# Optimization experiments

Measured on AMD Instinct MI355X. Metric: run time of the kernel, lower is better.

The kernel has to match this reference:

```python
import jax, jax.numpy as jnp
import numpy as np

B, S, DIM, H, DH, DEPTH, NCLS = 4, 2048, 128, 8, 128, 2, 10
M = 128          # number of FAVOR+ random features
CHUNK = 128      # chunk size for causal linear attention
INNER = H * DH   # performer-pytorch: dim_head=dim -> inner_dim = heads*dim
FF = 4 * DIM


def layernorm(x, g, b, eps=1e-5):
    mu = jnp.mean(x, axis=-1, keepdims=True)
    var = jnp.mean((x - mu) ** 2, axis=-1, keepdims=True)
    return (x - mu) * jax.lax.rsqrt(var + eps) * g + b


def softmax_kernel(data, proj, is_query, eps=1e-4):
    # FAVOR+ positive softmax-kernel features. data: [B,H,S,DH], proj: [M,DH]
    norm = DH ** -0.25
    ratio = M ** -0.5
    d = data * norm
    dd = jnp.einsum('bhsd,md->bhsm', d, proj)
    diag = 0.5 * jnp.sum(d * d, axis=-1, keepdims=True)
    if is_query:
        stab = jnp.max(dd, axis=-1, keepdims=True)
    else:
        stab = jnp.max(dd, axis=(-2, -1), keepdims=True)
    stab = jax.lax.stop_gradient(stab)
    return ratio * (jnp.exp(dd - diag - stab) + eps)


def causal_linear_attention(qp, kp, v):
    # qp,kp: [B,H,S,M], v: [B,H,S,DH]; chunked prefix-sum causal linear attention
    b, h, s, m = qp.shape
    d = v.shape[-1]
    nc = s // CHUNK
    def to_chunks(t):
        return t.reshape(b, h, nc, CHUNK, -1).transpose(2, 0, 1, 3, 4)
    qc, kc, vc = to_chunks(qp), to_chunks(kp), to_chunks(v)
    tri = jnp.tril(jnp.ones((CHUNK, CHUNK), qp.dtype))
    def step(carry, inp):
        kv_sum, k_sum = carry           # [b,h,m,d], [b,h,m]
        qi, ki, vi = inp                # [b,h,CHUNK,*]
        attn = jnp.einsum('bhim,bhjm->bhij', qi, ki) * tri
        num = jnp.einsum('bhij,bhjd->bhid', attn, vi) \
            + jnp.einsum('bhim,bhmd->bhid', qi, kv_sum)
        den = jnp.sum(attn, axis=-1) + jnp.einsum('bhim,bhm->bhi', qi, k_sum)
        out = num / (den[..., None] + 1e-6)
        kv_sum = kv_sum + jnp.einsum('bhjm,bhjd->bhmd', ki, vi)
        k_sum = k_sum + jnp.sum(ki, axis=2)
        return (kv_sum, k_sum), out
    init = (jnp.zeros((b, h, m, d), qp.dtype), jnp.zeros((b, h, m), qp.dtype))
    _, out = jax.lax.scan(step, init, (qc, kc, vc))
    return out.transpose(1, 2, 0, 3, 4).reshape(b, h, s, d)


def setup_inputs():
    key = jax.random.key(0)
    ks = jax.random.split(key, 12)
    rng = np.random.default_rng(0)
    # sinusoidal positional encoding [S, DIM]
    pe = np.zeros((S, DIM), np.float32)
    pos = np.arange(S)[:, None].astype(np.float32)
    div = np.exp(np.arange(0, DIM, 2).astype(np.float32) * (-np.log(10000.0) / DIM))
    pe[:, 0::2] = np.sin(pos * div)
    pe[:, 1::2] = np.cos(pos * div)
    # orthogonal random feature projections per layer [DEPTH, M, DH]
    proj = np.stack([
        (np.linalg.qr(rng.standard_normal((DH, DH)))[0][:M] * np.sqrt(DH))
        for _ in range(DEPTH)
    ]).astype(np.float32)
    def gn(k, shape, scale):
        return jax.random.normal(k, shape, jnp.float32) * scale
    return {
        'x': gn(ks[0], (B, S, 1), 1.0),
        'lin_w': gn(ks[1], (1, DIM), 1.0),
        'lin_b': jnp.zeros((DIM,), jnp.float32),
        'pe': jnp.asarray(pe),
        'proj': jnp.asarray(proj),
        'ln1_g': jnp.ones((DEPTH, DIM), jnp.float32),
        'ln1_b': jnp.zeros((DEPTH, DIM), jnp.float32),
        'wq': gn(ks[2], (DEPTH, DIM, INNER), DIM ** -0.5),
        'wk': gn(ks[3], (DEPTH, DIM, INNER), DIM ** -0.5),
        'wv': gn(ks[4], (DEPTH, DIM, INNER), DIM ** -0.5),
        'wo': gn(ks[5], (DEPTH, INNER, DIM), INNER ** -0.5),
        'wo_b': jnp.zeros((DEPTH, DIM), jnp.float32),
        'ln2_g': jnp.ones((DEPTH, DIM), jnp.float32),
        'ln2_b': jnp.zeros((DEPTH, DIM), jnp.float32),
        'ff1_w': gn(ks[6], (DEPTH, DIM, FF), DIM ** -0.5),
        'ff1_b': jnp.zeros((DEPTH, FF), jnp.float32),
        'ff2_w': gn(ks[7], (DEPTH, FF, DIM), FF ** -0.5),
        'ff2_b': jnp.zeros((DEPTH, DIM), jnp.float32),
        'fin_w': gn(ks[8], (DIM, NCLS), DIM ** -0.5),
        'fin_b': jnp.zeros((NCLS,), jnp.float32),
    }


def reference(x, lin_w, lin_b, pe, proj, ln1_g, ln1_b, wq, wk, wv, wo, wo_b,
              ln2_g, ln2_b, ff1_w, ff1_b, ff2_w, ff2_b, fin_w, fin_b):
    h = x @ lin_w + lin_b            # [B,S,DIM]
    h = h + pe[None]
    for l in range(DEPTH):
        # --- pre-norm FAVOR+ causal self-attention ---
        y = layernorm(h, ln1_g[l], ln1_b[l])
        def split(t):  # [B,S,INNER] -> [B,H,S,DH]
            return t.reshape(B, S, H, DH).transpose(0, 2, 1, 3)
        q, k, v = split(y @ wq[l]), split(y @ wk[l]), split(y @ wv[l])
        qp = softmax_kernel(q, proj[l], True)
        kp = softmax_kernel(k, proj[l], False)
        o = causal_linear_attention(qp, kp, v)          # [B,H,S,DH]
        o = o.transpose(0, 2, 1, 3).reshape(B, S, INNER)
        h = h + (o @ wo[l] + wo_b[l])
        # --- pre-norm FFN ---
        y = layernorm(h, ln2_g[l], ln2_b[l])
        f = jax.nn.gelu(y @ ff1_w[l] + ff1_b[l]) @ ff2_w[l] + ff2_b[l]
        h = h + f
    pooled = jnp.mean(h, axis=1)     # [B,DIM]
    return pooled @ fin_w + fin_b    # [B,NCLS]
```

## Files before the change

kernel.cpp:

```cpp
#include <hip/hip_runtime.h>
#include <hip/hip_bf16.h>

#define Bb 4
#define Ss 2048
#define DIMc 128
#define Hh 8
#define DHc 128
#define Mf 128
#define CH 128
#define NCc 16
#define INNERc 1024
#define FFc 512

union F4 { float4 v; float f[4]; };
typedef unsigned short u16;

typedef __bf16 bf16x8 __attribute__((ext_vector_type(8)));
typedef float  f32x4  __attribute__((ext_vector_type(4)));

__device__ __forceinline__ unsigned fkey(float f){
  unsigned b = __float_as_uint(f);
  return (b & 0x80000000u) ? ~b : (b | 0x80000000u);
}
__device__ __forceinline__ float funkey(unsigned u){
  unsigned b = (u & 0x80000000u) ? (u & 0x7fffffffu) : ~u;
  return __uint_as_float(b);
}
__device__ __forceinline__ float gelu_f(float x){
  return 0.5f*x*(1.0f + tanhf(0.7978845608028654f*(x + 0.044715f*x*x*x)));
}
__device__ __forceinline__ u16 f2bu(float f){
  unsigned u = __float_as_uint(f);
  return (u16)((u + 0x7fffu + ((u>>16)&1u)) >> 16);
}
__device__ __forceinline__ float b2f(u16 u){
  return __uint_as_float(((unsigned)u)<<16);
}

__device__ __forceinline__ bf16x8 ldfrag(const u16* base, int row, int e){
  int byte = (row*256 + e*2) ^ ((row&7)<<4);
  return *(const bf16x8*)((const char*)base + byte);
}
__device__ __forceinline__ void stage_lin_bf(u16* dst, const u16* src, int srs, int t){
  #pragma unroll
  for(int it=0; it<8; ++it){
    int idx = t + it*256; int r = idx>>4, c8 = idx&15;
    int byte = (r*256 + c8*16) ^ ((r&7)<<4);
    *(uint4*)((char*)dst + byte) = *(const uint4*)(src + r*srs + c8*8);
  }
}
__device__ __forceinline__ void stage_lin_bf_s(u16* dst, const u16* src, int srs,
    int t, float sc, float off){
  #pragma unroll
  for(int it=0; it<8; ++it){
    int idx = t + it*256; int r = idx>>4, c8 = idx&15;
    u16 tmp[8]; *(uint4*)tmp = *(const uint4*)(src + r*srs + c8*8);
    #pragma unroll
    for(int u=0;u<8;u++) tmp[u] = f2bu(fmaf(b2f(tmp[u]), sc, off));
    int byte = (r*256 + c8*16) ^ ((r&7)<<4);
    *(uint4*)((char*)dst + byte) = *(uint4*)tmp;
  }
}
__device__ __forceinline__ void stage_lin_f32(u16* dst, const float* src, int srs, int t){
  #pragma unroll
  for(int it=0; it<8; ++it){
    int idx = t + it*256; int r = idx>>4, c8 = idx&15;
    F4 v0, v1;
    v0.v = *(const float4*)(src + r*srs + c8*8);
    v1.v = *(const float4*)(src + r*srs + c8*8 + 4);
    u16 tmp[8];
    #pragma unroll
    for(int u=0;u<4;u++){ tmp[u] = f2bu(v0.f[u]); tmp[4+u] = f2bu(v1.f[u]); }
    int byte = (r*256 + c8*16) ^ ((r&7)<<4);
    *(uint4*)((char*)dst + byte) = *(uint4*)tmp;
  }
}
__device__ __forceinline__ void stage_tr_bf(u16* dst, const u16* src, int srs, int t){
  int j0 = (t & 63)*2; int wv = t>>6;
  #pragma unroll
  for(int it=0; it<2; ++it){
    int d0 = wv*16 + it*64;
    u16 a0[16], a1[16];
    *(uint4*)&a0[0] = *(const uint4*)(src + j0*srs + d0);
    *(uint4*)&a0[8] = *(const uint4*)(src + j0*srs + d0 + 8);
    *(uint4*)&a1[0] = *(const uint4*)(src + (j0+1)*srs + d0);
    *(uint4*)&a1[8] = *(const uint4*)(src + (j0+1)*srs + d0 + 8);
    #pragma unroll
    for(int dc=0; dc<16; ++dc){
      int d = d0 + dc;
      unsigned pk = (unsigned)a0[dc] | ((unsigned)a1[dc]<<16);
      int byte = (d*256 + j0*2) ^ ((d&7)<<4);
      *(unsigned*)((char*)dst + byte) = pk;
    }
  }
}
__device__ __forceinline__ void stage_tr_bf_s(u16* dst, const u16* src, int srs,
    int t, float sc, float off){
  int j0 = (t & 63)*2; int wv = t>>6;
  #pragma unroll
  for(int it=0; it<2; ++it){
    int d0 = wv*16 + it*64;
    u16 a0[16], a1[16];
    *(uint4*)&a0[0] = *(const uint4*)(src + j0*srs + d0);
    *(uint4*)&a0[8] = *(const uint4*)(src + j0*srs + d0 + 8);
    *(uint4*)&a1[0] = *(const uint4*)(src + (j0+1)*srs + d0);
    *(uint4*)&a1[8] = *(const uint4*)(src + (j0+1)*srs + d0 + 8);
    #pragma unroll
    for(int dc=0; dc<16; ++dc){
      int d = d0 + dc;
      unsigned pk = (unsigned)f2bu(fmaf(b2f(a0[dc]), sc, off)) |
                    ((unsigned)f2bu(fmaf(b2f(a1[dc]), sc, off))<<16);
      int byte = (d*256 + j0*2) ^ ((d&7)<<4);
      *(unsigned*)((char*)dst + byte) = pk;
    }
  }
}

__device__ __forceinline__ int2 swz_tile(){
  int nx = gridDim.x;
  int nwg = gridDim.x*gridDim.y;
  int lin = blockIdx.y*nx + blockIdx.x;
  int q = nwg>>3, r = nwg&7;
  int xcd = lin&7, idx = lin>>3;
  int nl = (xcd<r) ? (xcd*(q+1)+idx) : (r*(q+1)+(xcd-r)*q+idx);
  return make_int2(nl % nx, nl / nx);
}

__global__ __launch_bounds__(64) void k_init(unsigned* kstab){
  if(threadIdx.x < 64) kstab[threadIdx.x] = 0u;
}

__global__ __launch_bounds__(256) void k_embed(const float* __restrict__ x,
    const float* __restrict__ lw, const float* __restrict__ lb,
    const float* __restrict__ pe, float* __restrict__ h){
  int idx = blockIdx.x*256 + threadIdx.x;
  int d = idx & 127; int bs = idx >> 7; int s = bs & (Ss-1);
  h[idx] = x[bs]*lw[d] + lb[d] + pe[s*DIMc + d];
}

__global__ __launch_bounds__(256) void k_ln(const float* __restrict__ in,
    const float* __restrict__ g, const float* __restrict__ bta,
    u16* __restrict__ out){
  int wave = threadIdx.x >> 6; int lane = threadIdx.x & 63;
  int row = blockIdx.x*4 + wave;
  const float* r = in + row*DIMc;
  float x1 = r[lane], x2 = r[lane+64];
  float s = x1+x2, sq = x1*x1 + x2*x2;
  #pragma unroll
  for(int m=1;m<64;m<<=1){ s += __shfl_xor(s,m,64); sq += __shfl_xor(sq,m,64); }
  float mu = s * (1.0f/128.0f);
  float var = sq*(1.0f/128.0f) - mu*mu;
  float rs = rsqrtf(var + 1e-5f);
  out[row*DIMc+lane]    = f2bu((x1-mu)*rs*g[lane]+bta[lane]);
  out[row*DIMc+lane+64] = f2bu((x2-mu)*rs*g[lane+64]+bta[lane+64]);
}

template<bool BIAS, bool GELU, bool RES, bool OBF>
__global__ __launch_bounds__(256) void k_gemm_bf(const u16* __restrict__ A,
    const float* __restrict__ Bw, const float* __restrict__ bias,
    const float* __restrict__ resid, void* __restrict__ Cp, int N, int K){
  __shared__ u16 As[64][40];
  __shared__ u16 Bs[64][40];
  int2 tt = swz_tile();
  int n0 = tt.x*64, m0 = tt.y*64;
  int t = threadIdx.x; int wid = t>>6, lane = t&63;
  int wr = wid>>1, wc = wid&1;
  int fr = lane&15, kc = lane>>4;
  f32x4 acc[2][2] = {};
  for(int k0=0; k0<K; k0+=32){
    {
      int r = t>>2, c8 = t&3;
      *(uint4*)&As[r][c8*8] = *(const uint4*)(A + (m0+r)*K + k0 + c8*8);
    }
    {
      int n = t&63, c8 = t>>6;
      u16 tmp[8];
      #pragma unroll
      for(int j=0;j<8;j++) tmp[j] = f2bu(Bw[(k0 + c8*8 + j)*N + n0 + n]);
      *(uint4*)&Bs[n][c8*8] = *(uint4*)tmp;
    }
    __syncthreads();
    bf16x8 af[2], bf[2];
    #pragma unroll
    for(int i=0;i<2;i++) af[i] = *(const bf16x8*)&As[wr*32 + i*16 + fr][kc*8];
    #pragma unroll
    for(int j=0;j<2;j++) bf[j] = *(const bf16x8*)&Bs[wc*32 + j*16 + fr][kc*8];
    #pragma unroll
    for(int i=0;i<2;i++)
      #pragma unroll
      for(int j=0;j<2;j++)
        acc[i][j] = __builtin_amdgcn_mfma_f32_16x16x32_bf16(af[i], bf[j], acc[i][j], 0, 0, 0);
    __syncthreads();
  }
  #pragma unroll
  for(int i=0;i<2;i++){
    #pragma unroll
    for(int r=0;r<4;r++){
      int row = m0 + wr*32 + i*16 + kc*4 + r;
      #pragma unroll
      for(int j=0;j<2;j++){
        int col = n0 + wc*32 + j*16 + fr;
        float val = acc[i][j][r];
        if(BIAS) val += bias[col];
        if(GELU) val = gelu_f(val);
        if(RES)  val += resid[row*N+col];
        if(OBF) ((u16*)Cp)[row*N+col] = f2bu(val);
        else    ((float*)Cp)[row*N+col] = val;
      }
    }
  }
}

template<bool ISQ>
__global__ __launch_bounds__(256) void k_featm(
    const u16* xin, u16* qout, const float* __restrict__ proj, unsigned* kstab){
  __shared__ __align__(16) u16 xs[16384];
  __shared__ __align__(16) u16 ps[16384];
  __shared__ float diag_s[128];
  __shared__ unsigned hmax[8];
  int r0 = blockIdx.x*128;
  int t = threadIdx.x; int lane = t&63, w = t>>6;
  int fr = lane&15, kc = lane>>4;
  const float norm  = 0.29730177875068026f;
  const float ratio = 0.08838834764831845f;
  if(!ISQ && t<8) hmax[t] = 0u;
  stage_lin_bf(xs, xin + (size_t)r0*128, 128, t);
  stage_lin_f32(ps, proj, 128, t);
  {
    int r = t>>1, half = t&1;
    const u16* rp = xin + (size_t)(r0+r)*128 + half*64;
    float ss = 0.f;
    #pragma unroll
    for(int u4=0; u4<8; ++u4){
      u16 tmp[8]; *(uint4*)tmp = *(const uint4*)(rp + u4*8);
      #pragma unroll
      for(int u=0;u<8;u++){ float f = b2f(tmp[u]); ss += f*f; }
    }
    ss += __shfl_xor(ss, 1, 64);
    if(half==0) diag_s[r] = 0.5f*norm*norm*ss;
  }
  __syncthreads();
  f32x4 acc[2][8] = {};
  #pragma unroll
  for(int ks=0; ks<4; ++ks){
    bf16x8 a[2];
    #pragma unroll
    for(int i=0;i<2;i++) a[i] = ldfrag(xs, w*32+i*16+fr, ks*32+kc*8);
    bf16x8 bm[8];
    #pragma unroll
    for(int cb=0;cb<8;cb++) bm[cb] = ldfrag(ps, cb*16+fr, ks*32+kc*8);
    #pragma unroll
    for(int i=0;i<2;i++)
      #pragma unroll
      for(int cb=0;cb<8;cb++)
        acc[i][cb] = __builtin_amdgcn_mfma_f32_16x16x32_bf16(a[i], bm[cb], acc[i][cb], 0,0,0);
  }
  __syncthreads();
  #pragma unroll
  for(int i=0;i<2;i++){
    #pragma unroll
    for(int r=0;r<4;r++){
      int row = w*32 + i*16 + kc*4 + r;
      float dg = diag_s[row];
      float rmax = acc[i][0][r];
      #pragma unroll
      for(int cb=1;cb<8;cb++) rmax = fmaxf(rmax, acc[i][cb][r]);
      #pragma unroll
      for(int msk=1;msk<16;msk<<=1) rmax = fmaxf(rmax, __shfl_xor(rmax, msk, 64));
      if(ISQ){
        float base = -dg - norm*rmax;
        #pragma unroll
        for(int cb=0;cb<8;cb++){
          float val = ratio*(expf(fmaf(norm, acc[i][cb][r], base)) + 1e-4f);
          int byte = (row*256 + (cb*16+fr)*2) ^ ((row&7)<<4);
          *(u16*)((char*)xs + byte) = f2bu(val);
        }
      } else {
        if(fr==0) atomicMax(&hmax[row&7], fkey(norm*rmax));
        #pragma unroll
        for(int cb=0;cb<8;cb++){
          float val = expf(fmaf(norm, acc[i][cb][r], -dg));
          int byte = (row*256 + (cb*16+fr)*2) ^ ((row&7)<<4);
          *(u16*)((char*)xs + byte) = f2bu(val);
        }
      }
    }
  }
  __syncthreads();
  #pragma unroll
  for(int it=0; it<8; ++it){
    int idx = t + it*256; int r = idx>>4, c8 = idx&15;
    int byte = (r*256 + c8*16) ^ ((r&7)<<4);
    *(uint4*)(qout + (size_t)(r0+r)*128 + c8*8) = *(uint4*)((char*)xs + byte);
  }
  if(!ISQ){
    int b = r0 >> 14;
    if(t<8) atomicMax(&kstab[b*8 + t], hmax[t]);
  }
}

__global__ __launch_bounds__(256) void k_attn1m(const u16* __restrict__ kp,
    const u16* __restrict__ v, u16* __restrict__ kvc, float* __restrict__ ksc,
    const unsigned* __restrict__ kstab){
  __shared__ __align__(16) u16 kt[16384];
  __shared__ __align__(16) u16 vt[16384];
  int bc = blockIdx.x; int c = bc&15, bh = bc>>4, b = bh>>3, hh = bh&7;
  int t = threadIdx.x; int lane = t&63, w = t>>6;
  int fr = lane&15, kc = lane>>4;
  int s0 = c*128;
  const float ratio = 0.08838834764831845f;
  float stab = funkey(kstab[bh]);
  float csc = ratio * expf(-stab);
  float reps = ratio * 1e-4f;
  const u16* kb = kp + (size_t)((b*Ss+s0)*Hh + hh)*128;
  const u16* vb = v  + (size_t)((b*Ss+s0)*Hh + hh)*128;
  stage_tr_bf_s(kt, kb, 1024, t, csc, reps);
  stage_tr_bf(vt, vb, 1024, t);
  __syncthreads();
  f32x4 acc[2][8] = {};
  f32x4 ks[2] = {};
  bf16x8 bones;
  #pragma unroll
  for(int e=0;e<8;e++) bones[e] = (fr==0) ? (__bf16)1.0f : (__bf16)0.0f;
  #pragma unroll
  for(int js=0;js<4;js++){
    bf16x8 am[2];
    #pragma unroll
    for(int i=0;i<2;i++) am[i] = ldfrag(kt, w*32+i*16+fr, js*32+kc*8);
    bf16x8 bv[8];
    #pragma unroll
    for(int cb=0;cb<8;cb++) bv[cb] = ldfrag(vt, cb*16+fr, js*32+kc*8);
    #pragma unroll
    for(int i=0;i<2;i++){
      ks[i] = __builtin_amdgcn_mfma_f32_16x16x32_bf16(am[i], bones, ks[i], 0,0,0);
      #pragma unroll
      for(int cb=0;cb<8;cb++)
        acc[i][cb] = __builtin_amdgcn_mfma_f32_16x16x32_bf16(am[i], bv[cb], acc[i][cb], 0,0,0);
    }
  }
  u16* kvb = kvc + (size_t)bc*16384;
  #pragma unroll
  for(int i=0;i<2;i++){
    #pragma unroll
    for(int r=0;r<4;r++){
      int m = w*32 + i*16 + kc*4 + r;
      #pragma unroll
      for(int cb=0;cb<8;cb++) kvb[m*128 + cb*16 + fr] = f2bu(acc[i][cb][r]);
      if(fr==0) ksc[bc*128 + m] = ks[i][r];
    }
  }
}

__global__ __launch_bounds__(256) void k_prefix(unsigned* __restrict__ kvc){
  int bh = blockIdx.x >> 5; int pos = (blockIdx.x & 31)*256 + threadIdx.x;
  int base = bh*16*8192 + pos;
  float a0 = 0.f, a1 = 0.f;
  #pragma unroll
  for(int c=0;c<16;c++){
    unsigned pk = kvc[base + c*8192];
    float x0 = b2f((u16)pk), x1 = b2f((u16)(pk>>16));
    kvc[base + c*8192] = (unsigned)f2bu(a0) | ((unsigned)f2bu(a1)<<16);
    a0 += x0; a1 += x1;
  }
}
__global__ __launch_bounds__(256) void k_prefix_ks(float* __restrict__ ksc){
  int e = blockIdx.x*256 + threadIdx.x;
  int bh = e>>7, m = e&127;
  float a = 0.f;
  #pragma unroll
  for(int c=0;c<16;c++){
    int idx = (bh*16+c)*128 + m;
    float xv = ksc[idx]; ksc[idx] = a; a += xv;
  }
}

__global__ __launch_bounds__(256) void k_attn2m(const u16* __restrict__ qp,
    const u16* __restrict__ kp, const u16* __restrict__ v,
    const u16* __restrict__ kvc, const float* __restrict__ ksc,
    u16* __restrict__ o, const unsigned* __restrict__ kstab){
  __shared__ __align__(16) u16 qs[16384];
  __shared__ __align__(16) u16 bs[16384];
  __shared__ float ksum_s[128];
  int bc = blockIdx.x; int c = bc&15, bh = bc>>4, b = bh>>3, hh = bh&7;
  int t = threadIdx.x; int lane = t&63, w = t>>6;
  int fr = lane&15, kc = lane>>4;
  int s0 = c*128;
  const float ratio = 0.08838834764831845f;
  float stab = funkey(kstab[bh]);
  float csc = ratio * expf(-stab);
  float reps = ratio * 1e-4f;
  const u16* qb = qp + (size_t)((b*Ss+s0)*Hh + hh)*128;
  const u16* kb = kp + (size_t)((b*Ss+s0)*Hh + hh)*128;
  const u16* vb = v  + (size_t)((b*Ss+s0)*Hh + hh)*128;
  const u16* kvb = kvc + (size_t)bc*16384;
  stage_lin_bf(qs, qb, 1024, t);
  stage_lin_bf_s(bs, kb, 1024, t, csc, reps);
  if(t<128) ksum_s[t] = ksc[bc*128 + t];
  __syncthreads();
  bf16x8 aq[2][4];
  #pragma unroll
  for(int i=0;i<2;i++)
    #pragma unroll
    for(int ks=0;ks<4;ks++)
      aq[i][ks] = ldfrag(qs, w*32+i*16+fr, ks*32+kc*8);
  f32x4 sacc[2][8] = {};
  #pragma unroll
  for(int ks=0;ks<4;ks++){
    bf16x8 bk[8];
    #pragma unroll
    for(int cb=0;cb<8;cb++) bk[cb] = ldfrag(bs, cb*16+fr, ks*32+kc*8);
    #pragma unroll
    for(int i=0;i<2;i++)
      #pragma unroll
      for(int cb=0;cb<8;cb++)
        sacc[i][cb] = __builtin_amdgcn_mfma_f32_16x16x32_bf16(aq[i][ks], bk[cb], sacc[i][cb], 0,0,0);
  }
  __syncthreads();
  #pragma unroll
  for(int i=0;i<2;i++){
    #pragma unroll
    for(int cb=0;cb<8;cb++){
      #pragma unroll
      for(int r=0;r<4;r++){
        int prow = w*32 + i*16 + kc*4 + r;
        int pcol = cb*16 + fr;
        float pv = (pcol > prow) ? 0.f : sacc[i][cb][r];
        int byte = (prow*256 + pcol*2) ^ ((prow&7)<<4);
        *(u16*)((char*)qs + byte) = f2bu(pv);
      }
    }
  }
  stage_tr_bf(bs, vb, 1024, t);
  __syncthreads();
  f32x4 nacc[2][8] = {};
  f32x4 dacc[2] = {};
  bf16x8 bones;
  #pragma unroll
  for(int e=0;e<8;e++) bones[e] = (fr==0) ? (__bf16)1.0f : (__bf16)0.0f;
  #pragma unroll
  for(int js=0;js<4;js++){
    bf16x8 ap[2];
    #pragma unroll
    for(int i=0;i<2;i++) ap[i] = ldfrag(qs, w*32+i*16+fr, js*32+kc*8);
    bf16x8 bv[8];
    #pragma unroll
    for(int cb=0;cb<8;cb++) bv[cb] = ldfrag(bs, cb*16+fr, js*32+kc*8);
    #pragma unroll
    for(int i=0;i<2;i++){
      dacc[i] = __builtin_amdgcn_mfma_f32_16x16x32_bf16(ap[i], bones, dacc[i], 0,0,0);
      #pragma unroll
      for(int cb=0;cb<8;cb++)
        nacc[i][cb] = __builtin_amdgcn_mfma_f32_16x16x32_bf16(ap[i], bv[cb], nacc[i][cb], 0,0,0);
    }
  }
  __syncthreads();
  stage_tr_bf(bs, kvb, 128, t);
  __syncthreads();
  #pragma unroll
  for(int ms=0;ms<4;ms++){
    bf16x8 bkv[8];
    #pragma unroll
    for(int cb=0;cb<8;cb++) bkv[cb] = ldfrag(bs, cb*16+fr, ms*32+kc*8);
    bf16x8 bks;
    #pragma unroll
    for(int e=0;e<8;e++) bks[e] = (fr==0) ? (__bf16)ksum_s[ms*32+kc*8+e] : (__bf16)0.0f;
    #pragma unroll
    for(int i=0;i<2;i++){
      dacc[i] = __builtin_amdgcn_mfma_f32_16x16x32_bf16(aq[i][ms], bks, dacc[i], 0,0,0);
      #pragma unroll
      for(int cb=0;cb<8;cb++)
        nacc[i][cb] = __builtin_amdgcn_mfma_f32_16x16x32_bf16(aq[i][ms], bkv[cb], nacc[i][cb], 0,0,0);
    }
  }
  #pragma unroll
  for(int i=0;i<2;i++){
    #pragma unroll
    for(int r=0;r<4;r++){
      float den = __shfl(dacc[i][r], lane & 48, 64);
      float inv = 1.0f/(den + 1e-6f);
      int row = w*32 + i*16 + kc*4 + r;
      u16* ob = o + (size_t)((b*Ss+s0+row)*Hh + hh)*128;
      #pragma unroll
      for(int cb=0;cb<8;cb++)
        ob[cb*16 + fr] = f2bu(nacc[i][cb][r] * inv);
    }
  }
}

__global__ __launch_bounds__(256) void k_pool(const float* __restrict__ h,
    float* __restrict__ pw){
  __shared__ float part[256];
  int blk = blockIdx.x; int b = blk>>4, c = blk&15;
  int t = threadIdx.x; int half = t>>7;
  float s = 0.f;
  int s0 = c*128 + half*64;
  for(int si=s0; si<s0+64; ++si) s += h[(b*Ss+si)*128 + (t&127)];
  part[t] = s;
  __syncthreads();
  if(t<128) pw[blk*128 + t] = part[t] + part[t+128];
}
__global__ __launch_bounds__(128) void k_cls(const float* __restrict__ pw,
    const float* __restrict__ fw, const float* __restrict__ fb,
    float* __restrict__ out){
  __shared__ float pool_s[128];
  int b = blockIdx.x; int t = threadIdx.x;
  float s = 0.f;
  for(int c=0;c<16;c++) s += pw[(b*16+c)*128 + t];
  pool_s[t] = s * (1.0f/2048.0f);
  __syncthreads();
  if(t<10){
    float a = fb[t];
    for(int d=0; d<128; ++d) a += pool_s[d]*fw[d*10+t];
    out[b*10+t] = a;
  }
}

extern "C" void kernel_launch(void* const* d_in, const int* in_sizes, int n_in,
                              void* d_out, int out_size, void* d_ws, size_t ws_size,
                              hipStream_t stream){
  (void)in_sizes; (void)n_in; (void)out_size; (void)ws_size;
  const float* x     = (const float*)d_in[0];
  const float* lin_w = (const float*)d_in[1];
  const float* lin_b = (const float*)d_in[2];
  const float* pe    = (const float*)d_in[3];
  const float* proj  = (const float*)d_in[4];
  const float* ln1_g = (const float*)d_in[5];
  const float* ln1_b = (const float*)d_in[6];
  const float* wq    = (const float*)d_in[7];
  const float* wk    = (const float*)d_in[8];
  const float* wv    = (const float*)d_in[9];
  const float* wo    = (const float*)d_in[10];
  const float* wo_b  = (const float*)d_in[11];
  const float* ln2_g = (const float*)d_in[12];
  const float* ln2_b = (const float*)d_in[13];
  const float* ff1w  = (const float*)d_in[14];
  const float* ff1b  = (const float*)d_in[15];
  const float* ff2w  = (const float*)d_in[16];
  const float* ff2b  = (const float*)d_in[17];
  const float* finw  = (const float*)d_in[18];
  const float* finb  = (const float*)d_in[19];
  float* out = (float*)d_out;

  float* ws  = (float*)d_ws;
  float* h    = ws;
  u16*  y    = (u16*)(h + 1048576);
  u16*  q    = (u16*)(h + 1048576 + 524288);
  u16*  k    = q + 8388608;
  u16*  v    = k + 8388608;
  u16*  o    = v + 8388608;
  u16*  kvc  = o + 8388608;
  float* ksc  = (float*)(kvc + 8388608);
  float* pw   = ksc + 65536;
  unsigned* kstab = (unsigned*)(pw + 8192);

  k_init<<<1,64,0,stream>>>(kstab);
  k_embed<<<4096,256,0,stream>>>(x, lin_w, lin_b, pe, h);
  for(int l=0;l<2;l++){
    const float* projl = proj + l*Mf*DHc;
    k_ln<<<2048,256,0,stream>>>(h, ln1_g + l*DIMc, ln1_b + l*DIMc, y);
    k_gemm_bf<false,false,false,true><<<dim3(16,128),256,0,stream>>>(y, wq + l*DIMc*INNERc, nullptr, nullptr, q, INNERc, DIMc);
    k_gemm_bf<false,false,false,true><<<dim3(16,128),256,0,stream>>>(y, wk + l*DIMc*INNERc, nullptr, nullptr, k, INNERc, DIMc);
    k_gemm_bf<false,false,false,true><<<dim3(16,128),256,0,stream>>>(y, wv + l*DIMc*INNERc, nullptr, nullptr, v, INNERc, DIMc);
    k_featm<true><<<512,256,0,stream>>>(q, q, projl, nullptr);
    k_featm<false><<<512,256,0,stream>>>(k, k, projl, kstab + l*32);
    k_attn1m<<<512,256,0,stream>>>(k, v, kvc, ksc, kstab + l*32);
    k_prefix<<<1024,256,0,stream>>>((unsigned*)kvc);
    k_prefix_ks<<<16,256,0,stream>>>(ksc);
    k_attn2m<<<512,256,0,stream>>>(q, k, v, kvc, ksc, o, kstab + l*32);
    k_gemm_bf<true,false,true,false><<<dim3(2,128),256,0,stream>>>(o, wo + l*INNERc*DIMc, wo_b + l*DIMc, h, h, DIMc, INNERc);
    k_ln<<<2048,256,0,stream>>>(h, ln2_g + l*DIMc, ln2_b + l*DIMc, y);
    k_gemm_bf<true,true,false,true><<<dim3(8,128),256,0,stream>>>(y, ff1w + l*DIMc*FFc, ff1b + l*FFc, nullptr, q, FFc, DIMc);
    k_gemm_bf<true,false,true,false><<<dim3(2,128),256,0,stream>>>(q, ff2w + l*FFc*DIMc, ff2b + l*DIMc, h, h, DIMc, FFc);
  }
  k_pool<<<64,256,0,stream>>>(h, pw);
  k_cls<<<4,128,0,stream>>>(pw, finw, finb, out);
}
```

Baseline: 455.9 us.

## Fuse QKV projections into one 128x128-tile GEMM and merge prefix kernels

Adds a k_gemm128 kernel with 128x128 output tiles and a full K=128 slab staged once in LDS. It computes Q, K and V in a single launch by selecting the weight and output per column tile, and it also replaces the FF1 GEMM (with bias and GELU). The two prefix-sum kernels are merged into one launch, cutting launch count and improving A-tile reuse. The costs are larger shared memory per block (64KB), which may lower occupancy, and strided fp32 weight loads converted to bf16 inside the kernel.

```diff
diff --git a/kernel.cpp b/kernel.cpp
--- a/kernel.cpp
+++ b/kernel.cpp
@@ -153,6 +153,70 @@
   float rs = rsqrtf(var + 1e-5f);
   out[row*DIMc+lane]    = f2bu((x1-mu)*rs*g[lane]+bta[lane]);
   out[row*DIMc+lane+64] = f2bu((x2-mu)*rs*g[lane+64]+bta[lane+64]);
+}
+
+template<bool QKV3, bool BIAS, bool GELU>
+__global__ __launch_bounds__(256) void k_gemm128(const u16* __restrict__ A,
+    const float* __restrict__ B0, const float* __restrict__ B1,
+    const float* __restrict__ B2, const float* __restrict__ bias,
+    u16* __restrict__ C0, u16* __restrict__ C1, u16* __restrict__ C2,
+    int N){
+  __shared__ __align__(16) u16 As[16384];
+  __shared__ __align__(16) u16 Bs[16384];
+  int2 tt = swz_tile();
+  int tn = tt.x, m0 = tt.y*128;
+  const float* Bw; u16* C; int n0;
+  if(QKV3){
+    int tpw = N>>7;
+    int widx = tn / tpw; n0 = (tn % tpw)*128;
+    Bw = (widx==0) ? B0 : ((widx==1) ? B1 : B2);
+    C  = (widx==0) ? C0 : ((widx==1) ? C1 : C2);
+  } else { Bw = B0; C = C0; n0 = tn*128; }
+  int t = threadIdx.x; int lane = t&63, w = t>>6;
+  int fr = lane&15, kc = lane>>4;
+  stage_lin_bf(As, A + (size_t)m0*128, 128, t);
+  {
+    #pragma unroll
+    for(int it=0; it<8; ++it){
+      int idx = t + it*256; int n = idx&127, c8 = idx>>7;
+      u16 tmp[8];
+      #pragma unroll
+      for(int j=0;j<8;j++) tmp[j] = f2bu(Bw[(c8*8+j)*N + n0 + n]);
+      int byte = (n*256 + c8*16) ^ ((n&7)<<4);
+      *(uint4*)((char*)Bs + byte) = *(uint4*)tmp;
+    }
+  }
+  __syncthreads();
+  f32x4 acc[2][8] = {};
+  #pragma unroll
+  for(int ks=0; ks<4; ++ks){
+    bf16x8 a[2];
+    #pragma unroll
+    for(int i=0;i<2;i++) a[i] = ldfrag(As, w*32+i*16+fr, ks*32+kc*8);
+    bf16x8 bm[8];
+    #pragma unroll
+    for(int cb=0;cb<8;cb++) bm[cb] = ldfrag(Bs, cb*16+fr, ks*32+kc*8);
+    #pragma unroll
+    for(int i=0;i<2;i++)
+      #pragma unroll
+      for(int cb=0;cb<8;cb++)
+        acc[i][cb] = __builtin_amdgcn_mfma_f32_16x16x32_bf16(a[i], bm[cb], acc[i][cb], 0,0,0);
+  }
+  #pragma unroll
+  for(int i=0;i<2;i++){
+    #pragma unroll
+    for(int r=0;r<4;r++){
+      int row = m0 + w*32 + i*16 + kc*4 + r;
+      #pragma unroll
+      for(int cb=0;cb<8;cb++){
+        int col = n0 + cb*16 + fr;
+        float val = acc[i][cb][r];
+        if(BIAS) val += bias[col];
+        if(GELU) val = gelu_f(val);
+        C[(size_t)row*N + col] = f2bu(val);
+      }
+    }
+  }
 }
 
 template<bool BIAS, bool GELU, bool RES, bool OBF>
@@ -351,26 +415,29 @@
   }
 }
 
-__global__ __launch_bounds__(256) void k_prefix(unsigned* __restrict__ kvc){
-  int bh = blockIdx.x >> 5; int pos = (blockIdx.x & 31)*256 + threadIdx.x;
-  int base = bh*16*8192 + pos;
-  float a0 = 0.f, a1 = 0.f;
-  #pragma unroll
-  for(int c=0;c<16;c++){
-    unsigned pk = kvc[base + c*8192];
-    float x0 = b2f((u16)pk), x1 = b2f((u16)(pk>>16));
-    kvc[base + c*8192] = (unsigned)f2bu(a0) | ((unsigned)f2bu(a1)<<16);
-    a0 += x0; a1 += x1;
-  }
-}
-__global__ __launch_bounds__(256) void k_prefix_ks(float* __restrict__ ksc){
-  int e = blockIdx.x*256 + threadIdx.x;
-  int bh = e>>7, m = e&127;
-  float a = 0.f;
-  #pragma unroll
-  for(int c=0;c<16;c++){
-    int idx = (bh*16+c)*128 + m;
-    float xv = ksc[idx]; ksc[idx] = a; a += xv;
+__global__ __launch_bounds__(256) void k_prefix2(unsigned* __restrict__ kvc,
+    float* __restrict__ ksc){
+  int blk = blockIdx.x;
+  if(blk < 1024){
+    int bh = blk >> 5; int pos = (blk & 31)*256 + threadIdx.x;
+    int base = bh*16*8192 + pos;
+    float a0 = 0.f, a1 = 0.f;
+    #pragma unroll
+    for(int c=0;c<16;c++){
+      unsigned pk = kvc[base + c*8192];
+      float x0 = b2f((u16)pk), x1 = b2f((u16)(pk>>16));
+      kvc[base + c*8192] = (unsigned)f2bu(a0) | ((unsigned)f2bu(a1)<<16);
+      a0 += x0; a1 += x1;
+    }
+  } else {
+    int e = (blk-1024)*256 + threadIdx.x;
+    int bh = e>>7, m = e&127;
+    float a = 0.f;
+    #pragma unroll
+    for(int c=0;c<16;c++){
+      int idx = (bh*16+c)*128 + m;
+      float xv = ksc[idx]; ksc[idx] = a; a += xv;
+    }
   }
 }
 
@@ -558,18 +625,19 @@
   for(int l=0;l<2;l++){
     const float* projl = proj + l*Mf*DHc;
     k_ln<<<2048,256,0,stream>>>(h, ln1_g + l*DIMc, ln1_b + l*DIMc, y);
-    k_gemm_bf<false,false,false,true><<<dim3(16,128),256,0,stream>>>(y, wq + l*DIMc*INNERc, nullptr, nullptr, q, INNERc, DIMc);
-    k_gemm_bf<false,false,false,true><<<dim3(16,128),256,0,stream>>>(y, wk + l*DIMc*INNERc, nullptr, nullptr, k, INNERc, DIMc);
-    k_gemm_bf<false,false,false,true><<<dim3(16,128),256,0,stream>>>(y, wv + l*DIMc*INNERc, nullptr, nullptr, v, INNERc, DIMc);
+    k_gemm128<true,false,false><<<dim3(24,64),256,0,stream>>>(
+        y, wq + l*DIMc*INNERc, wk + l*DIMc*INNERc, wv + l*DIMc*INNERc,
+        nullptr, q, k, v, INNERc);
     k_featm<true><<<512,256,0,stream>>>(q, q, projl, nullptr);
     k_featm<false><<<512,256,0,stream>>>(k, k, projl, kstab + l*32);
     k_attn1m<<<512,256,0,stream>>>(k, v, kvc, ksc, kstab + l*32);
-    k_prefix<<<1024,256,0,stream>>>((unsigned*)kvc);
-    k_prefix_ks<<<16,256,0,stream>>>(ksc);
+    k_prefix2<<<1040,256,0,stream>>>((unsigned*)kvc, ksc);
     k_attn2m<<<512,256,0,stream>>>(q, k, v, kvc, ksc, o, kstab + l*32);
     k_gemm_bf<true,false,true,false><<<dim3(2,128),256,0,stream>>>(o, wo + l*INNERc*DIMc, wo_b + l*DIMc, h, h, DIMc, INNERc);
     k_ln<<<2048,256,0,stream>>>(h, ln2_g + l*DIMc, ln2_b + l*DIMc, y);
-    k_gemm_bf<true,true,false,true><<<dim3(8,128),256,0,stream>>>(y, ff1w + l*DIMc*FFc, ff1b + l*FFc, nullptr, q, FFc, DIMc);
+    k_gemm128<false,true,true><<<dim3(4,64),256,0,stream>>>(
+        y, ff1w + l*DIMc*FFc, nullptr, nullptr, ff1b + l*FFc,
+        q, nullptr, nullptr, FFc);
     k_gemm_bf<true,false,true,false><<<dim3(2,128),256,0,stream>>>(q, ff2w + l*FFc*DIMc, ff2b + l*DIMc, h, h, DIMc, FFc);
   }
   k_pool<<<64,256,0,stream>>>(h, pw);
```

Result: faster. 438.1 us (-3.9%).
